# Performance work log

Hardware: AMD Instinct MI355X
Metric: run time of the kernel (lower is better)

The kernel has to match this reference:

```python
import jax, jax.numpy as jnp
import numpy as np

V, D, H, HS, BLK, L = 50257, 768, 12, 64, 1024, 6
B, S = 4, 1024
EPS = 1e-5


def layer_norm(x, g, b):
    mu = jnp.mean(x, axis=-1, keepdims=True)
    var = jnp.mean(jnp.square(x - mu), axis=-1, keepdims=True)
    return (x - mu) * jax.lax.rsqrt(var + EPS) * g + b


def setup_inputs() -> dict:
    key = jax.random.key(0)
    ks = jax.random.split(key, 24)
    s = 0.02
    inp = {
        "idx": jax.random.randint(ks[0], (B, S), 0, V),
        "tok_emb": jax.random.normal(ks[1], (V, D), jnp.float32) * s,
        "pos_emb": jax.random.normal(ks[2], (BLK, D), jnp.float32) * s,
        "Wq": jax.random.normal(ks[3], (L, H, D, HS), jnp.float32) * s,
        "bq": jnp.zeros((L, H, HS), jnp.float32),
        "Wk": jax.random.normal(ks[4], (L, H, D, HS), jnp.float32) * s,
        "bk": jnp.zeros((L, H, HS), jnp.float32),
        "Wv": jax.random.normal(ks[5], (L, H, D, HS), jnp.float32) * s,
        "bv": jnp.zeros((L, H, HS), jnp.float32),
        "Wproj": jax.random.normal(ks[6], (L, D, D), jnp.float32) * s,
        "bproj": jnp.zeros((L, D), jnp.float32),
        "ln1_g": jnp.ones((L, D), jnp.float32),
        "ln1_b": jnp.zeros((L, D), jnp.float32),
        "ln2_g": jnp.ones((L, D), jnp.float32),
        "ln2_b": jnp.zeros((L, D), jnp.float32),
        "Wf1": jax.random.normal(ks[7], (L, D, 4 * D), jnp.float32) * s,
        "bf1": jnp.zeros((L, 4 * D), jnp.float32),
        "Wf2": jax.random.normal(ks[8], (L, 4 * D, D), jnp.float32) * s,
        "bf2": jnp.zeros((L, D), jnp.float32),
        "lnf_g": jnp.ones((D,), jnp.float32),
        "lnf_b": jnp.zeros((D,), jnp.float32),
        "Wlm": jax.random.normal(ks[9], (V, D), jnp.float32) * s,
    }
    return inp


def attention(x, Wq, bq, Wk, bk, Wv, bv, Wproj, bproj):
    # x: [B,S,D]; per-head projections stacked over H
    q = jnp.einsum("bsd,hdk->bhsk", x, Wq) + bq[:, None, :]
    k = jnp.einsum("bsd,hdk->bhsk", x, Wk) + bk[:, None, :]
    v = jnp.einsum("bsd,hdk->bhsk", x, Wv) + bv[:, None, :]
    scores = jnp.einsum("bhsk,bhtk->bhst", q, k)  # [B,H,S,S]
    s = x.shape[1]
    mask = jnp.tril(jnp.ones((s, s), bool))
    # original: masked_fill(-inf) THEN divide by sqrt(head_size) -- equivalent
    scores = jnp.where(mask, scores, -jnp.inf) / np.sqrt(HS)
    w = jax.nn.softmax(scores, axis=-1)
    out = jnp.einsum("bhst,bhtk->bhsk", w, v)
    out = out.transpose(0, 2, 1, 3).reshape(x.shape[0], s, H * HS)
    return out @ Wproj + bproj


def reference(idx, tok_emb, pos_emb, Wq, bq, Wk, bk, Wv, bv, Wproj, bproj,
              ln1_g, ln1_b, ln2_g, ln2_b, Wf1, bf1, Wf2, bf2, lnf_g, lnf_b, Wlm):
    s = idx.shape[1]
    x = tok_emb[idx] + pos_emb[:s]
    for i in range(L):
        h = layer_norm(x, ln1_g[i], ln1_b[i])
        x = x + attention(h, Wq[i], bq[i], Wk[i], bk[i], Wv[i], bv[i], Wproj[i], bproj[i])
        h = layer_norm(x, ln2_g[i], ln2_b[i])
        x = x + (jax.nn.gelu(h @ Wf1[i] + bf1[i], approximate=False) @ Wf2[i] + bf2[i])
    x = layer_norm(x, lnf_g, lnf_b)
    logits = x @ Wlm.T  # [B,S,V]
    return logits
```

## Files before the change

kernel.cpp:

```cpp
#include <hip/hip_runtime.h>
#include <hip/hip_bf16.h>
#include <math.h>

#define D_MODEL 768
#define N_HEAD  12
#define HEAD    64
#define SEQ     1024
#define NLAYER  6
#define BATCH   4
#define NROWS   (BATCH*SEQ)
#define VOCAB   50257
#define VPAD    50432
#define DFFN    3072
#define DQKV    2304

typedef __attribute__((ext_vector_type(8))) __bf16 bf16x8;
typedef __attribute__((ext_vector_type(4))) float f32x4;
typedef __attribute__((ext_vector_type(4))) unsigned short u16x4;
typedef __attribute__((ext_vector_type(8))) unsigned short u16x8;

__device__ inline unsigned short f2bf(float x) {
    __hip_bfloat16 h = __float2bfloat16(x);
    return *reinterpret_cast<unsigned short*>(&h);
}

__global__ __launch_bounds__(256)
void embed_ln_kernel(const int* __restrict__ idx, const float* __restrict__ tok,
                     const float* __restrict__ pos, const float* __restrict__ gw,
                     const float* __restrict__ bw, float* __restrict__ x,
                     unsigned short* __restrict__ hb) {
    int row = blockIdx.x;
    int t = idx[row];
    int s = row & (SEQ - 1);
    int tid = threadIdx.x;
    const float* tp = tok + (size_t)t * D_MODEL;
    const float* pp = pos + (size_t)s * D_MODEL;
    float v0 = tp[tid]       + pp[tid];
    float v1 = tp[tid + 256] + pp[tid + 256];
    float v2 = tp[tid + 512] + pp[tid + 512];
    float* xp = x + (size_t)row * D_MODEL;
    xp[tid] = v0; xp[tid + 256] = v1; xp[tid + 512] = v2;
    float sm  = v0 + v1 + v2;
    float sq = v0*v0 + v1*v1 + v2*v2;
    #pragma unroll
    for (int o = 1; o < 64; o <<= 1) { sm += __shfl_xor(sm, o); sq += __shfl_xor(sq, o); }
    __shared__ float red[8];
    int wave = tid >> 6;
    if ((tid & 63) == 0) { red[wave] = sm; red[4 + wave] = sq; }
    __syncthreads();
    sm = red[0] + red[1] + red[2] + red[3];
    sq = red[4] + red[5] + red[6] + red[7];
    float mean = sm * (1.0f / D_MODEL);
    float var  = sq * (1.0f / D_MODEL) - mean * mean;
    float rstd = rsqrtf(var + 1e-5f);
    unsigned short* op = hb + (size_t)row * D_MODEL;
    op[tid]       = f2bf((v0 - mean) * rstd * gw[tid]       + bw[tid]);
    op[tid + 256] = f2bf((v1 - mean) * rstd * gw[tid + 256] + bw[tid + 256]);
    op[tid + 512] = f2bf((v2 - mean) * rstd * gw[tid + 512] + bw[tid + 512]);
}

__global__ __launch_bounds__(256)
void ln_kernel(const float* __restrict__ in, const float* __restrict__ gw,
               const float* __restrict__ bw, unsigned short* __restrict__ out) {
    int row = blockIdx.x;
    int tid = threadIdx.x;
    const float* x = in + (size_t)row * D_MODEL;
    float v0 = x[tid], v1 = x[tid + 256], v2 = x[tid + 512];
    float s  = v0 + v1 + v2;
    float sq = v0*v0 + v1*v1 + v2*v2;
    #pragma unroll
    for (int o = 1; o < 64; o <<= 1) { s += __shfl_xor(s, o); sq += __shfl_xor(sq, o); }
    __shared__ float red[8];
    int wave = tid >> 6;
    if ((tid & 63) == 0) { red[wave] = s; red[4 + wave] = sq; }
    __syncthreads();
    s  = red[0] + red[1] + red[2] + red[3];
    sq = red[4] + red[5] + red[6] + red[7];
    float mean = s * (1.0f / D_MODEL);
    float var  = sq * (1.0f / D_MODEL) - mean * mean;
    float rstd = rsqrtf(var + 1e-5f);
    unsigned short* op = out + (size_t)row * D_MODEL;
    op[tid]       = f2bf((v0 - mean) * rstd * gw[tid]       + bw[tid]);
    op[tid + 256] = f2bf((v1 - mean) * rstd * gw[tid + 256] + bw[tid + 256]);
    op[tid + 512] = f2bf((v2 - mean) * rstd * gw[tid + 512] + bw[tid + 512]);
}

template<int MODE>
__global__ __launch_bounds__(256)
void conv_transpose(const float* __restrict__ in, unsigned short* __restrict__ out,
                    int K, int N, size_t inLstride, size_t outLstride) {
    __shared__ float t[64][65];
    const int tid = threadIdx.x;
    const int n0 = blockIdx.x * 64, k0 = blockIdx.y * 64;
    const float* ip = in + blockIdx.z * inLstride;
    unsigned short* op = out + blockIdx.z * outLstride;
    {
        const int kk = tid >> 4, nq = tid & 15;
        #pragma unroll
        for (int p = 0; p < 4; ++p) {
            int k = kk + p * 16;
            float4 v;
            if (MODE == 0) v = *reinterpret_cast<const float4*>(&ip[(size_t)(k0 + k) * N + n0 + nq * 4]);
            else           v = *reinterpret_cast<const float4*>(&ip[((size_t)(n0 >> 6) * K + (k0 + k)) * 64 + nq * 4]);
            t[k][nq * 4 + 0] = v.x; t[k][nq * 4 + 1] = v.y;
            t[k][nq * 4 + 2] = v.z; t[k][nq * 4 + 3] = v.w;
        }
    }
    __syncthreads();
    {
        const int n = tid >> 2, kq = tid & 3;
        unsigned short buf[16];
        #pragma unroll
        for (int j = 0; j < 16; ++j) buf[j] = f2bf(t[kq * 16 + j][n]);
        unsigned short* dst = &op[(size_t)(n0 + n) * K + k0 + kq * 16];
        *reinterpret_cast<u16x8*>(dst)     = *reinterpret_cast<u16x8*>(&buf[0]);
        *reinterpret_cast<u16x8*>(dst + 8) = *reinterpret_cast<u16x8*>(&buf[8]);
    }
}

__global__ __launch_bounds__(256)
void conv_lm(const float* __restrict__ in, unsigned short* __restrict__ out) {
    const int nchunks = VPAD * D_MODEL / 4;
    const int vchunks = VOCAB * D_MODEL / 4;
    for (int i = blockIdx.x * 256 + threadIdx.x; i < nchunks; i += gridDim.x * 256) {
        u16x4 o;
        if (i < vchunks) {
            float4 v = reinterpret_cast<const float4*>(in)[i];
            o[0] = f2bf(v.x); o[1] = f2bf(v.y); o[2] = f2bf(v.z); o[3] = f2bf(v.w);
        } else { o[0] = 0; o[1] = 0; o[2] = 0; o[3] = 0; }
        reinterpret_cast<u16x4*>(out)[i] = o;
    }
}

__global__ __launch_bounds__(256)
void conv_bias(const float* __restrict__ bq, const float* __restrict__ bk,
               const float* __restrict__ bv, float* __restrict__ out) {
    int i = blockIdx.x * 256 + threadIdx.x;
    if (i >= NLAYER * DQKV) return;
    int l = i / DQKV, n = i % DQKV;
    float v;
    if (n < 768)        v = bq[l * 768 + n];
    else if (n < 1536)  v = bk[l * 768 + n - 768];
    else                v = bv[l * 768 + n - 1536];
    out[i] = v;
}

__global__ __launch_bounds__(512)
void gemm256_mfma(const unsigned short* __restrict__ A, const unsigned short* __restrict__ B,
                  float* __restrict__ C, int M, int N, int K) {
    __shared__ unsigned short smem[2 * 2 * 16384];
    const int nwg = gridDim.x;
    const int t0 = (blockIdx.x & 7) * (nwg >> 3) + (blockIdx.x >> 3);
    const int MT = M >> 8;
    const int NBX = nwg / MT;
    const int srsize = NBX * 8;
    const int sr = t0 / srsize;
    const int rem = t0 - sr * srsize;
    const int bx = rem >> 3;
    const int by = sr * 8 + (rem & 7);
    const int bm = by * 256, bn = bx * 256;
    const int tid = threadIdx.x;
    const int l = tid & 63, w = tid >> 6;
    const int wm = w >> 2, wn = w & 3;
    const int lr = l & 15, lc = l >> 4;
    f32x4 acc[8][4] = {};

    auto stage = [&](int k0, int buf) {
        #pragma unroll
        for (int p = 0; p < 4; ++p) {
            int d16 = p * 512 + tid;
            int row = d16 >> 3, cph = d16 & 7;
            int clog = cph ^ (row & 7);
            const unsigned short* ga = A + (size_t)(bm + row) * K + k0 + clog * 8;
            __builtin_amdgcn_global_load_lds(
                (const __attribute__((address_space(1))) unsigned int*)ga,
                (__attribute__((address_space(3))) unsigned int*)(&smem[buf * 32768 + d16 * 8]), 16, 0, 0);
        }
        #pragma unroll
        for (int p = 0; p < 4; ++p) {
            int d16 = p * 512 + tid;
            int row = d16 >> 3, cph = d16 & 7;
            int clog = cph ^ (row & 7);
            const unsigned short* gb = B + (size_t)(bn + row) * K + k0 + clog * 8;
            __builtin_amdgcn_global_load_lds(
                (const __attribute__((address_space(1))) unsigned int*)gb,
                (__attribute__((address_space(3))) unsigned int*)(&smem[buf * 32768 + 16384 + d16 * 8]), 16, 0, 0);
        }
    };

    auto compute = [&](int buf) {
        const unsigned short* Ab = &smem[buf * 32768];
        const unsigned short* Bb = &smem[buf * 32768 + 16384];
        bf16x8 bfr[2][4];
        #pragma unroll
        for (int ks = 0; ks < 2; ++ks)
            #pragma unroll
            for (int j = 0; j < 4; ++j) {
                int col = wn * 64 + j * 16 + lr;
                bfr[ks][j] = *reinterpret_cast<const bf16x8*>(
                    &Bb[col * 64 + (((ks * 4 + lc) ^ (col & 7)) * 8)]);
            }
        #pragma unroll
        for (int qm = 0; qm < 2; ++qm) {
            bf16x8 af[2][4];
            #pragma unroll
            for (int ks = 0; ks < 2; ++ks)
                #pragma unroll
                for (int mi = 0; mi < 4; ++mi) {
                    int row = wm * 128 + qm * 64 + mi * 16 + lr;
                    af[ks][mi] = *reinterpret_cast<const bf16x8*>(
                        &Ab[row * 64 + (((ks * 4 + lc) ^ (row & 7)) * 8)]);
                }
            __builtin_amdgcn_s_setprio(1);
            #pragma unroll
            for (int ks = 0; ks < 2; ++ks)
                #pragma unroll
                for (int mi = 0; mi < 4; ++mi)
                    #pragma unroll
                    for (int j = 0; j < 4; ++j)
                        acc[qm * 4 + mi][j] = __builtin_amdgcn_mfma_f32_16x16x32_bf16(
                            bfr[ks][j], af[ks][mi], acc[qm * 4 + mi][j], 0, 0, 0);
            __builtin_amdgcn_s_setprio(0);
        }
    };

    const int NT = K >> 6;
    stage(0, 0);
    asm volatile("s_waitcnt vmcnt(0)" ::: "memory");
    __builtin_amdgcn_s_barrier();
    for (int t = 0; t < NT; ++t) {
        const int cur = t & 1;
        if (t + 1 < NT) stage((t + 1) << 6, cur ^ 1);
        compute(cur);
        if (t + 1 < NT) {
            asm volatile("s_waitcnt vmcnt(0)" ::: "memory");
            __builtin_amdgcn_s_barrier();
        }
    }

    #pragma unroll
    for (int i = 0; i < 8; ++i) {
        const int row = bm + wm * 128 + i * 16 + lr;
        #pragma unroll
        for (int j = 0; j < 4; ++j) {
            const int colb = bn + wn * 64 + j * 16 + lc * 4;
            if (colb + 3 < N) {
                *reinterpret_cast<f32x4*>(&C[(size_t)row * N + colb]) = acc[i][j];
            } else {
                #pragma unroll
                for (int r = 0; r < 4; ++r)
                    if (colb + r < N) C[(size_t)row * N + colb + r] = acc[i][j][r];
            }
        }
    }
}

template<int BN, int OUTF , bool GELU, bool RES>
__global__ __launch_bounds__(256)
void gemm_sched(const unsigned short* __restrict__ A, const unsigned short* __restrict__ B,
                const float* __restrict__ bias, const float* __restrict__ res,
                void* __restrict__ Cout, int M, int N, int K) {
    constexpr int ABUF = 64 * 64;
    constexpr int TBUF = (64 + BN) * 64;
    constexpr int NI = BN / 32;
    __shared__ unsigned short smem[2 * TBUF];
    const int nwg = gridDim.x;
    const int t0 = (blockIdx.x & 7) * (nwg >> 3) + (blockIdx.x >> 3);
    const int MT = M >> 6;
    const int NBX = nwg / MT;
    const int srsize = NBX * 8;
    const int sr = t0 / srsize;
    const int rem = t0 - sr * srsize;
    const int bx = rem >> 3;
    const int by = sr * 8 + (rem & 7);
    const int bm = by * 64, bn = bx * BN;
    const int tid = threadIdx.x;
    const int l = tid & 63, w = tid >> 6;
    const int wr = (w & 1) * 32;
    const int wc = (w >> 1) * (BN / 2);
    const int lr = l & 15, lc = l >> 4;
    f32x4 acc[2][NI] = {};

    auto stage = [&](int k0, int buf) {
        #pragma unroll
        for (int p = 0; p < 2; ++p) {
            int d16 = p * 256 + tid;
            int row = d16 >> 3, cph = d16 & 7;
            int clog = cph ^ (row & 7);
            const unsigned short* ga = A + (size_t)(bm + row) * K + k0 + clog * 8;
            __builtin_amdgcn_global_load_lds(
                (const __attribute__((address_space(1))) unsigned int*)ga,
                (__attribute__((address_space(3))) unsigned int*)(&smem[buf * TBUF + d16 * 8]), 16, 0, 0);
        }
        #pragma unroll
        for (int p = 0; p < BN / 32; ++p) {
            int d16 = p * 256 + tid;
            int row = d16 >> 3, cph = d16 & 7;
            int clog = cph ^ (row & 7);
            const unsigned short* gb = B + (size_t)(bn + row) * K + k0 + clog * 8;
            __builtin_amdgcn_global_load_lds(
                (const __attribute__((address_space(1))) unsigned int*)gb,
                (__attribute__((address_space(3))) unsigned int*)(&smem[buf * TBUF + ABUF + d16 * 8]), 16, 0, 0);
        }
    };

    auto compute = [&](int buf) {
        const unsigned short* Ab = &smem[buf * TBUF];
        const unsigned short* Bb = &smem[buf * TBUF + ABUF];
        #pragma unroll
        for (int ks = 0; ks < 2; ++ks) {
            bf16x8 af[2], bfr[NI];
            #pragma unroll
            for (int mi = 0; mi < 2; ++mi) {
                int row = wr + mi * 16 + lr;
                af[mi] = *reinterpret_cast<const bf16x8*>(
                    &Ab[row * 64 + (((ks * 4 + lc) ^ (row & 7)) * 8)]);
            }
            #pragma unroll
            for (int ni = 0; ni < NI; ++ni) {
                int col = wc + ni * 16 + lr;
                bfr[ni] = *reinterpret_cast<const bf16x8*>(
                    &Bb[col * 64 + (((ks * 4 + lc) ^ (col & 7)) * 8)]);
            }
            __builtin_amdgcn_s_setprio(1);
            #pragma unroll
            for (int mi = 0; mi < 2; ++mi)
                #pragma unroll
                for (int ni = 0; ni < NI; ++ni)
                    acc[mi][ni] = __builtin_amdgcn_mfma_f32_16x16x32_bf16(
                        bfr[ni], af[mi], acc[mi][ni], 0, 0, 0);
            __builtin_amdgcn_s_setprio(0);
        }
    };

    const int NT = K >> 6;
    stage(0, 0);
    asm volatile("s_waitcnt vmcnt(0)" ::: "memory");
    __builtin_amdgcn_s_barrier();
    for (int t = 0; t < NT; ++t) {
        const int cur = t & 1;
        if (t + 1 < NT) stage((t + 1) << 6, cur ^ 1);
        compute(cur);
        if (t + 1 < NT) {
            asm volatile("s_waitcnt vmcnt(0)" ::: "memory");
            __builtin_amdgcn_s_barrier();
        }
    }

    #pragma unroll
    for (int mi = 0; mi < 2; ++mi) {
        const int row = bm + wr + mi * 16 + lr;
        #pragma unroll
        for (int ni = 0; ni < NI; ++ni) {
            const int colb = bn + wc + ni * 16 + lc * 4;
            f32x4 v = acc[mi][ni];
            if (bias) v += *reinterpret_cast<const f32x4*>(&bias[colb]);
            if (GELU) {
                #pragma unroll
                for (int r = 0; r < 4; ++r)
                    v[r] = 0.5f * v[r] * (1.0f + erff(v[r] * 0.70710678118654752f));
            }
            if (RES) v += *reinterpret_cast<const f32x4*>(&res[(size_t)row * N + colb]);
            if (OUTF == 0) {
                *reinterpret_cast<f32x4*>(&((float*)Cout)[(size_t)row * N + colb]) = v;
            } else {
                u16x4 o;
                o[0] = f2bf(v[0]); o[1] = f2bf(v[1]); o[2] = f2bf(v[2]); o[3] = f2bf(v[3]);
                *reinterpret_cast<u16x4*>(&((unsigned short*)Cout)[(size_t)row * N + colb]) = o;
            }
        }
    }
}

__global__ __launch_bounds__(512)
void attn_mfma(const unsigned short* __restrict__ qkv, unsigned short* __restrict__ ao) {
    const int qt = gridDim.x - 1 - blockIdx.x;
    const int h = blockIdx.y, b = blockIdx.z;
    const int tid = threadIdx.x;
    const int w = tid >> 6, l = tid & 63;
    const int c = l & 15, g = l >> 4;

    __shared__ unsigned short Ks[2][32 * 64];
    __shared__ unsigned short Vt[2][64 * 40];
    __shared__ unsigned int   Ps[8][16 * 20];

    const unsigned short* base = qkv + (size_t)(b * SEQ) * DQKV + h * HEAD;
    const int q0 = qt * 128 + w * 16;

    bf16x8 qf[2];
    {
        const unsigned short* qp = base + (size_t)(q0 + c) * DQKV + g * 8;
        qf[0] = *reinterpret_cast<const bf16x8*>(qp);
        qf[1] = *reinterpret_cast<const bf16x8*>(qp + 32);
    }

    f32x4 o_acc[4] = {};
    float m_run[4]  = {-INFINITY, -INFINITY, -INFINITY, -INFINITY};
    float l_run[4]  = {0.f, 0.f, 0.f, 0.f};

    const int srow = tid >> 4, sch8 = tid & 15;
    const int scj = sch8 >> 1, sh = sch8 & 1;
    const int vd = tid & 63, vw = tid >> 6;

    u16x4 kreg;
    unsigned short vreg[4];
    auto loadKV = [&](int kt) {
        kreg = *reinterpret_cast<const u16x4*>(
            base + (size_t)(kt * 32 + srow) * DQKV + 768 + sch8 * 4);
        #pragma unroll
        for (int j = 0; j < 4; ++j)
            vreg[j] = base[(size_t)(kt * 32 + vw * 4 + j) * DQKV + 1536 + vd];
    };

    const int nkt = 4 * qt + 4;
    loadKV(0);
    for (int kt = 0; kt < nkt; ++kt) {
        const int bf = kt & 1;
        *reinterpret_cast<u16x4*>(&Ks[bf][srow * 64 + ((scj ^ (srow & 7)) * 8) + sh * 4]) = kreg;
        {
            uint2 pk;
            pk.x = vreg[0] | ((unsigned)vreg[1] << 16);
            pk.y = vreg[2] | ((unsigned)vreg[3] << 16);
            *reinterpret_cast<uint2*>(&Vt[bf][vd * 40 + vw * 4]) = pk;
        }
        __syncthreads();
        if (kt + 1 < nkt) loadKV(kt + 1);

        f32x4 s_acc[2] = {};
        #pragma unroll
        for (int t = 0; t < 2; ++t) {
            const int kr = t * 16 + c;
            #pragma unroll
            for (int ks = 0; ks < 2; ++ks) {
                bf16x8 kf = *reinterpret_cast<const bf16x8*>(
                    &Ks[bf][kr * 64 + (((ks * 4 + g) ^ (kr & 7)) * 8)]);
                s_acc[t] = __builtin_amdgcn_mfma_f32_16x16x32_bf16(qf[ks], kf, s_acc[t], 0, 0, 0);
            }
        }
        float sc[2][4];
        #pragma unroll
        for (int t = 0; t < 2; ++t) {
            const int kglob = kt * 32 + t * 16 + c;
            #pragma unroll
            for (int r = 0; r < 4; ++r) {
                float v = s_acc[t][r] * 0.125f;
                sc[t][r] = (kglob > q0 + g * 4 + r) ? -1e30f : v;
            }
        }
        float pout[2][4];
        #pragma unroll
        for (int r = 0; r < 4; ++r) {
            float tmax = fmaxf(sc[0][r], sc[1][r]);
            #pragma unroll
            for (int ms = 1; ms < 16; ms <<= 1) tmax = fmaxf(tmax, __shfl_xor(tmax, ms));
            float mnew = fmaxf(m_run[r], tmax);
            float alpha = __expf(m_run[r] - mnew);
            float p0 = __expf(sc[0][r] - mnew);
            float p1 = __expf(sc[1][r] - mnew);
            float psum = p0 + p1;
            #pragma unroll
            for (int ms = 1; ms < 16; ms <<= 1) psum += __shfl_xor(psum, ms);
            l_run[r] = l_run[r] * alpha + psum;
            m_run[r] = mnew;
            #pragma unroll
            for (int dt = 0; dt < 4; ++dt) o_acc[dt][r] *= alpha;
            pout[0][r] = p0; pout[1][r] = p1;
        }
        #pragma unroll
        for (int t = 0; t < 2; ++t) {
            #pragma unroll
            for (int r = 0; r < 4; ++r) {
                int my = f2bf(pout[t][r]);
                int part = __shfl_xor(my, 1);
                unsigned int word = (c & 1) ? ((unsigned)(part & 0xffff) | ((unsigned)my << 16))
                                            : ((unsigned)(my & 0xffff) | ((unsigned)part << 16));
                Ps[w][(g * 4 + r) * 20 + t * 8 + (c >> 1)] = word;
            }
        }
        uint4 praw = *reinterpret_cast<const uint4*>(&Ps[w][c * 20 + g * 4]);
        bf16x8 pf = *reinterpret_cast<const bf16x8*>(&praw);
        #pragma unroll
        for (int dt = 0; dt < 4; ++dt) {
            bf16x8 vf = *reinterpret_cast<const bf16x8*>(&Vt[bf][(dt * 16 + c) * 40 + g * 8]);
            o_acc[dt] = __builtin_amdgcn_mfma_f32_16x16x32_bf16(pf, vf, o_acc[dt], 0, 0, 0);
        }
    }

    float inv[4];
    #pragma unroll
    for (int r = 0; r < 4; ++r) inv[r] = 1.0f / l_run[r];
    #pragma unroll
    for (int r = 0; r < 4; ++r) {
        unsigned short* op = ao + (size_t)(b * SEQ + q0 + g * 4 + r) * D_MODEL + h * HEAD + c;
        #pragma unroll
        for (int dt = 0; dt < 4; ++dt)
            op[dt * 16] = f2bf(o_acc[dt][r] * inv[r]);
    }
}

extern "C" void kernel_launch(void* const* d_in, const int* in_sizes, int n_in,
                              void* d_out, int out_size, void* d_ws, size_t ws_size,
                              hipStream_t stream) {
    const int*   idx     = (const int*)  d_in[0];
    const float* tok_emb = (const float*)d_in[1];
    const float* pos_emb = (const float*)d_in[2];
    const float* Wq      = (const float*)d_in[3];
    const float* bq      = (const float*)d_in[4];
    const float* Wk      = (const float*)d_in[5];
    const float* bk      = (const float*)d_in[6];
    const float* Wv      = (const float*)d_in[7];
    const float* bv      = (const float*)d_in[8];
    const float* Wproj   = (const float*)d_in[9];
    const float* bproj   = (const float*)d_in[10];
    const float* ln1g    = (const float*)d_in[11];
    const float* ln1b    = (const float*)d_in[12];
    const float* ln2g    = (const float*)d_in[13];
    const float* ln2b    = (const float*)d_in[14];
    const float* Wf1     = (const float*)d_in[15];
    const float* bf1     = (const float*)d_in[16];
    const float* Wf2     = (const float*)d_in[17];
    const float* bf2     = (const float*)d_in[18];
    const float* lnfg    = (const float*)d_in[19];
    const float* lnfb    = (const float*)d_in[20];
    const float* Wlm     = (const float*)d_in[21];
    float* outp = (float*)d_out;

    char* basep = (char*)d_ws;
    size_t off = 0;
    auto alloc = [&](size_t bytes) -> void* {
        void* p = basep + off;
        off = (off + bytes + 255) & ~(size_t)255;
        return p;
    };
    float*          x      = (float*)         alloc((size_t)NROWS * D_MODEL * 4);
    unsigned short* qkv    = (unsigned short*)alloc((size_t)NROWS * DQKV * 2);
    unsigned short* hb     = (unsigned short*)alloc((size_t)NROWS * D_MODEL * 2);
    unsigned short* ao     = (unsigned short*)alloc((size_t)NROWS * D_MODEL * 2);
    unsigned short* mid    = (unsigned short*)alloc((size_t)NROWS * DFFN * 2);
    unsigned short* Wqkvb  = (unsigned short*)alloc((size_t)NLAYER * DQKV * D_MODEL * 2);
    unsigned short* Wprojb = (unsigned short*)alloc((size_t)NLAYER * D_MODEL * D_MODEL * 2);
    unsigned short* Wf1b   = (unsigned short*)alloc((size_t)NLAYER * DFFN * D_MODEL * 2);
    unsigned short* Wf2b   = (unsigned short*)alloc((size_t)NLAYER * D_MODEL * DFFN * 2);
    unsigned short* Wlmb   = (unsigned short*)alloc((size_t)VPAD * D_MODEL * 2);
    float*          bqkv   = (float*)         alloc((size_t)NLAYER * DQKV * 4);

    dim3 blk(256);

    conv_lm<<<2048, blk, 0, stream>>>(Wlm, Wlmb);
    conv_transpose<1><<<dim3(12, 12, 6), blk, 0, stream>>>(Wq, Wqkvb,             768, 768,  (size_t)768*768,  (size_t)DQKV*768);
    conv_transpose<1><<<dim3(12, 12, 6), blk, 0, stream>>>(Wk, Wqkvb + 768*768,   768, 768,  (size_t)768*768,  (size_t)DQKV*768);
    conv_transpose<1><<<dim3(12, 12, 6), blk, 0, stream>>>(Wv, Wqkvb + 2*768*768, 768, 768,  (size_t)768*768,  (size_t)DQKV*768);
    conv_transpose<0><<<dim3(12, 12, 6), blk, 0, stream>>>(Wproj, Wprojb,         768, 768,  (size_t)768*768,  (size_t)768*768);
    conv_transpose<0><<<dim3(48, 12, 6), blk, 0, stream>>>(Wf1, Wf1b,             768, 3072, (size_t)768*3072, (size_t)3072*768);
    conv_transpose<0><<<dim3(12, 48, 6), blk, 0, stream>>>(Wf2, Wf2b,             3072, 768, (size_t)3072*768, (size_t)768*3072);
    conv_bias<<<(NLAYER * DQKV + 255) / 256, blk, 0, stream>>>(bq, bk, bv, bqkv);

    embed_ln_kernel<<<NROWS, blk, 0, stream>>>(idx, tok_emb, pos_emb, ln1g, ln1b, x, hb);

    dim3 gqkv(64 * 18);
    dim3 g768s(64 * 12);
    dim3 g3072(64 * 24);
    dim3 ga(SEQ / 128, N_HEAD, BATCH);

    for (int li = 0; li < NLAYER; ++li) {
        if (li > 0)
            ln_kernel<<<NROWS, blk, 0, stream>>>(x, ln1g + li * D_MODEL, ln1b + li * D_MODEL, hb);

        gemm_sched<128, 1, false, false><<<gqkv, blk, 0, stream>>>(
            hb, Wqkvb + (size_t)li * DQKV * D_MODEL, bqkv + li * DQKV, nullptr,
            qkv, NROWS, DQKV, D_MODEL);

        attn_mfma<<<ga, dim3(512), 0, stream>>>(qkv, ao);

        gemm_sched<64, 0, false, true><<<g768s, blk, 0, stream>>>(
            ao, Wprojb + (size_t)li * D_MODEL * D_MODEL, bproj + li * D_MODEL, x,
            x, NROWS, D_MODEL, D_MODEL);

        ln_kernel<<<NROWS, blk, 0, stream>>>(x, ln2g + li * D_MODEL, ln2b + li * D_MODEL, hb);

        gemm_sched<128, 1, true, false><<<g3072, blk, 0, stream>>>(
            hb, Wf1b + (size_t)li * DFFN * D_MODEL, bf1 + li * DFFN, nullptr,
            mid, NROWS, DFFN, D_MODEL);

        gemm_sched<64, 0, false, true><<<g768s, blk, 0, stream>>>(
            mid, Wf2b + (size_t)li * D_MODEL * DFFN, bf2 + li * D_MODEL, x,
            x, NROWS, D_MODEL, DFFN);
    }

    ln_kernel<<<NROWS, blk, 0, stream>>>(x, lnfg, lnfb, hb);

    dim3 gl((VPAD / 256) * (NROWS / 256));
    gemm256_mfma<<<gl, dim3(512), 0, stream>>>(hb, Wlmb, outp, NROWS, VOCAB, D_MODEL);
}
```

Baseline: 1.928 ms.

## Split GEMM K-tiles into half-stages with fine-grained interleaved load/MFMA pipeline

Restructures the 256x256 bf16 MFMA GEMM main loop so each 64-wide K tile is staged as two 32-wide halves per matrix, with a new XOR swizzle for 32-element rows. Global-to-LDS loads for upcoming half-tiles are issued between MFMA phases, and partial vmcnt waits let several loads stay in flight instead of draining everything each tile. The goal is to overlap memory traffic with compute more tightly and shrink exposed load latency. It adds many more barriers per iteration and assumes NT is even.

```diff
diff --git a/kernel.cpp b/kernel.cpp
--- a/kernel.cpp
+++ b/kernel.cpp
@@ -148,7 +148,7 @@
 __global__ __launch_bounds__(512)
 void gemm256_mfma(const unsigned short* __restrict__ A, const unsigned short* __restrict__ B,
                   float* __restrict__ C, int M, int N, int K) {
-    __shared__ unsigned short smem[2 * 2 * 16384];
+    __shared__ unsigned short smem[65536];
     const int nwg = gridDim.x;
     const int t0 = (blockIdx.x & 7) * (nwg >> 3) + (blockIdx.x >> 3);
     const int MT = M >> 8;
@@ -165,77 +165,98 @@
     const int lr = l & 15, lc = l >> 4;
     f32x4 acc[8][4] = {};
 
-    auto stage = [&](int k0, int buf) {
-        #pragma unroll
-        for (int p = 0; p < 4; ++p) {
-            int d16 = p * 512 + tid;
-            int row = d16 >> 3, cph = d16 & 7;
-            int clog = cph ^ (row & 7);
-            const unsigned short* ga = A + (size_t)(bm + row) * K + k0 + clog * 8;
+    auto stageHalf = [&](int tile, int mat, int S) {
+        const unsigned short* G = mat ? B : A;
+        const int gbase = mat ? bn : bm;
+        unsigned short* dst = &smem[(tile & 1) * 32768 + mat * 16384 + S * 8192];
+        const int k0 = (tile << 6) + S * 32;
+        #pragma unroll
+        for (int p = 0; p < 2; ++p) {
+            int u = p * 512 + tid;
+            int row = u >> 2, qp = u & 3;
+            int ql = qp ^ ((row >> 1) & 3);
+            const unsigned short* g = G + (size_t)(gbase + row) * K + k0 + ql * 8;
             __builtin_amdgcn_global_load_lds(
-                (const __attribute__((address_space(1))) unsigned int*)ga,
-                (__attribute__((address_space(3))) unsigned int*)(&smem[buf * 32768 + d16 * 8]), 16, 0, 0);
-        }
-        #pragma unroll
-        for (int p = 0; p < 4; ++p) {
-            int d16 = p * 512 + tid;
-            int row = d16 >> 3, cph = d16 & 7;
-            int clog = cph ^ (row & 7);
-            const unsigned short* gb = B + (size_t)(bn + row) * K + k0 + clog * 8;
-            __builtin_amdgcn_global_load_lds(
-                (const __attribute__((address_space(1))) unsigned int*)gb,
-                (__attribute__((address_space(3))) unsigned int*)(&smem[buf * 32768 + 16384 + d16 * 8]), 16, 0, 0);
+                (const __attribute__((address_space(1))) unsigned int*)g,
+                (__attribute__((address_space(3))) unsigned int*)(&dst[u * 8]), 16, 0, 0);
         }
     };
-
-    auto compute = [&](int buf) {
-        const unsigned short* Ab = &smem[buf * 32768];
-        const unsigned short* Bb = &smem[buf * 32768 + 16384];
-        bf16x8 bfr[2][4];
-        #pragma unroll
-        for (int ks = 0; ks < 2; ++ks)
-            #pragma unroll
-            for (int j = 0; j < 4; ++j) {
-                int col = wn * 64 + j * 16 + lr;
-                bfr[ks][j] = *reinterpret_cast<const bf16x8*>(
-                    &Bb[col * 64 + (((ks * 4 + lc) ^ (col & 7)) * 8)]);
-            }
-        #pragma unroll
-        for (int qm = 0; qm < 2; ++qm) {
-            bf16x8 af[2][4];
-            #pragma unroll
-            for (int ks = 0; ks < 2; ++ks)
-                #pragma unroll
-                for (int mi = 0; mi < 4; ++mi) {
-                    int row = wm * 128 + qm * 64 + mi * 16 + lr;
-                    af[ks][mi] = *reinterpret_cast<const bf16x8*>(
-                        &Ab[row * 64 + (((ks * 4 + lc) ^ (row & 7)) * 8)]);
-                }
-            __builtin_amdgcn_s_setprio(1);
-            #pragma unroll
-            for (int ks = 0; ks < 2; ++ks)
-                #pragma unroll
-                for (int mi = 0; mi < 4; ++mi)
-                    #pragma unroll
-                    for (int j = 0; j < 4; ++j)
-                        acc[qm * 4 + mi][j] = __builtin_amdgcn_mfma_f32_16x16x32_bf16(
-                            bfr[ks][j], af[ks][mi], acc[qm * 4 + mi][j], 0, 0, 0);
-            __builtin_amdgcn_s_setprio(0);
+    auto readA4 = [&](int buf, int S, int mh, bf16x8* af) {
+        const unsigned short* Ab = &smem[buf * 32768 + S * 8192];
+        #pragma unroll
+        for (int mi = 0; mi < 4; ++mi) {
+            int R = wm * 128 + mh * 64 + mi * 16 + lr;
+            af[mi] = *reinterpret_cast<const bf16x8*>(&Ab[R * 32 + ((lc ^ ((R >> 1) & 3)) * 8)]);
         }
     };
+    auto readB4 = [&](int buf, int S, bf16x8* bfr) {
+        const unsigned short* Bb = &smem[buf * 32768 + 16384 + S * 8192];
+        #pragma unroll
+        for (int ni = 0; ni < 4; ++ni) {
+            int R = wn * 64 + ni * 16 + lr;
+            bfr[ni] = *reinterpret_cast<const bf16x8*>(&Bb[R * 32 + ((lc ^ ((R >> 1) & 3)) * 8)]);
+        }
+    };
 
     const int NT = K >> 6;
-    stage(0, 0);
+    stageHalf(0, 0, 0); stageHalf(0, 1, 0); stageHalf(0, 0, 1); stageHalf(0, 1, 1);
+    stageHalf(1, 0, 0); stageHalf(1, 1, 0);
     asm volatile("s_waitcnt vmcnt(0)" ::: "memory");
     __builtin_amdgcn_s_barrier();
-    for (int t = 0; t < NT; ++t) {
-        const int cur = t & 1;
-        if (t + 1 < NT) stage((t + 1) << 6, cur ^ 1);
-        compute(cur);
-        if (t + 1 < NT) {
-            asm volatile("s_waitcnt vmcnt(0)" ::: "memory");
+
+    for (int i = 0; i < (NT >> 1); ++i) {
+        const int T0 = 2 * i, T1 = T0 + 1;
+        const bool lastit = (T0 + 2 >= NT);
+        bf16x8 af[4], bfr[4];
+
+        auto mfma16 = [&](int mh) {
+            __builtin_amdgcn_s_setprio(1);
+            #pragma unroll
+            for (int mi = 0; mi < 4; ++mi)
+                #pragma unroll
+                for (int ni = 0; ni < 4; ++ni)
+                    acc[mh * 4 + mi][ni] = __builtin_amdgcn_mfma_f32_16x16x32_bf16(
+                        bfr[ni], af[mi], acc[mh * 4 + mi][ni], 0, 0, 0);
+            __builtin_amdgcn_s_setprio(0);
+        };
+        auto phend = [&]() {
+            if (lastit) asm volatile("s_waitcnt vmcnt(0)" ::: "memory");
+            else        asm volatile("s_waitcnt vmcnt(8)" ::: "memory");
             __builtin_amdgcn_s_barrier();
-        }
+        };
+
+        readB4(0, 0, bfr); readA4(0, 0, 0, af);
+        stageHalf(T1, 0, 1);
+        __builtin_amdgcn_s_barrier();
+        mfma16(0); phend();
+        readA4(0, 0, 1, af);
+        stageHalf(T1, 1, 1);
+        __builtin_amdgcn_s_barrier();
+        mfma16(1); phend();
+        readB4(0, 1, bfr); readA4(0, 1, 0, af);
+        if (!lastit) stageHalf(T0 + 2, 0, 0);
+        __builtin_amdgcn_s_barrier();
+        mfma16(0); phend();
+        readA4(0, 1, 1, af);
+        if (!lastit) stageHalf(T0 + 2, 1, 0);
+        __builtin_amdgcn_s_barrier();
+        mfma16(1); phend();
+        readB4(1, 0, bfr); readA4(1, 0, 0, af);
+        if (!lastit) stageHalf(T0 + 2, 0, 1);
+        __builtin_amdgcn_s_barrier();
+        mfma16(0); phend();
+        readA4(1, 0, 1, af);
+        if (!lastit) stageHalf(T0 + 2, 1, 1);
+        __builtin_amdgcn_s_barrier();
+        mfma16(1); phend();
+        readB4(1, 1, bfr); readA4(1, 1, 0, af);
+        if (!lastit) stageHalf(T1 + 2, 0, 0);
+        __builtin_amdgcn_s_barrier();
+        mfma16(0); phend();
+        readA4(1, 1, 1, af);
+        if (!lastit) stageHalf(T1 + 2, 1, 0);
+        __builtin_amdgcn_s_barrier();
+        mfma16(1); phend();
     }
 
     #pragma unroll
```

New measurement: 1.970 ms. 1.02x slower.
